# Performance work log

Hardware: AMD Instinct MI355X
Metric: run time of the kernel (lower is better)

## Reference

```python
import jax, jax.numpy as jnp
import numpy as np

N, E, G = 32768, 262144, 512
IN_DIM, HID, HEADS = 300, 128, 4
D_FUSED = HID * HEADS  # 512
L = 3


def setup_inputs() -> dict:
    key = jax.random.key(0)
    ks = jax.random.split(key, 24)
    s = 0.02
    inp = {
        "x": jax.random.normal(ks[0], (N, IN_DIM), jnp.float32),
        "edge_index": jax.random.randint(ks[1], (2, E), 0, N, jnp.int32),
        "batch": jnp.sort(jax.random.randint(ks[2], (N,), 0, G, jnp.int32)),
        "syn_w": jax.random.normal(ks[3], (IN_DIM, HID)) * s,
        "syn_b": jnp.zeros((HID,), jnp.float32),
        "ant_w": jax.random.normal(ks[4], (IN_DIM, HID)) * s,
        "ant_b": jnp.zeros((HID,), jnp.float32),
        "fusion_w": jax.random.normal(ks[5], (2 * HID, D_FUSED)) * s,
        "fusion_b": jnp.zeros((D_FUSED,), jnp.float32),
        "Wq": jax.random.normal(ks[6], (L, D_FUSED, D_FUSED)) * s,
        "bq": jnp.zeros((L, D_FUSED), jnp.float32),
        "Wk": jax.random.normal(ks[7], (L, D_FUSED, D_FUSED)) * s,
        "bk": jnp.zeros((L, D_FUSED), jnp.float32),
        "Wv": jax.random.normal(ks[8], (L, D_FUSED, D_FUSED)) * s,
        "bv": jnp.zeros((L, D_FUSED), jnp.float32),
        "Wskip": jax.random.normal(ks[9], (L, D_FUSED, D_FUSED)) * s,
        "bskip": jnp.zeros((L, D_FUSED), jnp.float32),
        "cls_w1": jax.random.normal(ks[10], (D_FUSED, HID)) * s,
        "cls_b1": jnp.zeros((HID,), jnp.float32),
        "cls_w2": jax.random.normal(ks[11], (HID, 1)) * s,
        "cls_b2": jnp.zeros((1,), jnp.float32),
    }
    return inp


def _transformer_conv(h, src, dst, Wq, bq, Wk, bk, Wv, bv, Wskip, bskip):
    # PyG TransformerConv: per-edge dot-product attention, softmax over in-neighbors of dst,
    # concat heads, plus root/skip linear (root_weight=True, concat=True, no edge_attr).
    n = h.shape[0]
    q = (h @ Wq + bq).reshape(n, HEADS, HID)
    k = (h @ Wk + bk).reshape(n, HEADS, HID)
    v = (h @ Wv + bv).reshape(n, HEADS, HID)
    scale = 1.0 / np.sqrt(HID)
    logits = jnp.einsum("ehd,ehd->eh", q[dst], k[src]) * scale  # [E, H]
    m = jax.ops.segment_max(logits, dst, num_segments=n)        # [N, H]
    e = jnp.exp(logits - m[dst])
    z = jax.ops.segment_sum(e, dst, num_segments=n)
    alpha = e / (z[dst] + 1e-16)                                # [E, H]
    msg = alpha[:, :, None] * v[src]                            # [E, H, D]
    out = jax.ops.segment_sum(msg, dst, num_segments=n).reshape(n, D_FUSED)
    return out + h @ Wskip + bskip


def reference(x, edge_index, batch, syn_w, syn_b, ant_w, ant_b, fusion_w, fusion_b,
              Wq, bq, Wk, bk, Wv, bv, Wskip, bskip, cls_w1, cls_b1, cls_w2, cls_b2):
    x_syn = jax.nn.relu(x @ syn_w + syn_b)
    x_ant = jax.nn.relu(x @ ant_w + ant_b)
    h = jnp.concatenate([x_syn, x_ant], axis=1) @ fusion_w + fusion_b  # [N, 512]
    src, dst = edge_index[0], edge_index[1]
    for l in range(L):
        h = jax.nn.relu(_transformer_conv(h, src, dst, Wq[l], bq[l], Wk[l], bk[l],
                                          Wv[l], bv[l], Wskip[l], bskip[l]))
    cnt = jax.ops.segment_sum(jnp.ones((h.shape[0],), h.dtype), batch, num_segments=G)
    pooled = jax.ops.segment_sum(h, batch, num_segments=G) / jnp.maximum(cnt, 1.0)[:, None]
    hid = jax.nn.relu(pooled @ cls_w1 + cls_b1)
    out = jax.nn.sigmoid(hid @ cls_w2 + cls_b2)
    return out.squeeze()
```

## Files before the change

kernel.cpp:

```cpp
#include <hip/hip_runtime.h>
#include <hip/hip_bf16.h>
#include <hip/hip_fp8.h>
#include <math.h>

#define N_NODES 32768
#define N_EDGES 262144
#define N_GRAPHS 512
#define IN_DIM 300
#define KPAD 320
#define HID 128
#define HEADS 4
#define D_FUSED 512
#define N_LAYERS 3

typedef __hip_bfloat16 bf16;
typedef short bf16x8 __attribute__((ext_vector_type(8)));
typedef short bf16x4 __attribute__((ext_vector_type(4)));
typedef float f32x4 __attribute__((ext_vector_type(4)));
typedef float f32x2 __attribute__((ext_vector_type(2)));

__device__ __forceinline__ float bfs_to_f(short s)
{
    unsigned u = ((unsigned)(unsigned short)s) << 16;
    return __builtin_bit_cast(float, u);
}

__device__ __forceinline__ short f_to_bfs(float v)
{
    return (short)__builtin_bit_cast(unsigned short, __float2bfloat16(v));
}

__device__ __forceinline__ void bf8_to_f32(bf16x8 v, float* f)
{
#pragma unroll
    for (int j = 0; j < 8; ++j) f[j] = bfs_to_f(v[j]);
}

__device__ __forceinline__ unsigned char f32_to_fp8(float v)
{
#if __has_builtin(__builtin_amdgcn_cvt_pk_fp8_f32)
    int p = __builtin_amdgcn_cvt_pk_fp8_f32(v, v, 0, false);
    return (unsigned char)(p & 0xff);
#else
    __hip_fp8_e4m3 t(v);
    return (unsigned char)t.__x;
#endif
}

__device__ __forceinline__ void fp8x8_to_f32(uint2 w, float* f)
{
#if __has_builtin(__builtin_amdgcn_cvt_pk_f32_fp8)
    f32x2 a = __builtin_amdgcn_cvt_pk_f32_fp8((int)w.x, false);
    f32x2 b = __builtin_amdgcn_cvt_pk_f32_fp8((int)w.x, true);
    f32x2 c = __builtin_amdgcn_cvt_pk_f32_fp8((int)w.y, false);
    f32x2 d = __builtin_amdgcn_cvt_pk_f32_fp8((int)w.y, true);
    f[0] = a.x; f[1] = a.y; f[2] = b.x; f[3] = b.y;
    f[4] = c.x; f[5] = c.y; f[6] = d.x; f[7] = d.y;
#else
    const unsigned char* p = (const unsigned char*)&w;
#pragma unroll
    for (int j = 0; j < 8; ++j) {
        __hip_fp8_e4m3 t;
        t.__x = (__hip_fp8_storage_t)p[j];
        f[j] = (float)t;
    }
#endif
}

__device__ __forceinline__ void gload_lds16(const void* g, void* l)
{
    __builtin_amdgcn_global_load_lds(
        (const __attribute__((address_space(1))) void*)g,
        (__attribute__((address_space(3))) void*)l, 16, 0, 0);
}

template <int K, int ACT, int EPI>
__global__ __launch_bounds__(512, 4) void mfma_gemm128(
    const bf16* __restrict__ A, int lda,
    const bf16* __restrict__ Bt,
    const float* __restrict__ bias,
    bf16* __restrict__ C0, int ldc0,
    bf16* __restrict__ C1, int ldc1, int csplit,
    unsigned char* __restrict__ C2,
    int nbx)
{
    __shared__ __align__(16) char lds[49152];

    const int t = threadIdx.x;
    const int wid = t >> 6, lane = t & 63;
    const int hi = lane >> 4, li = lane & 15;
    const int wr = wid >> 2, wc = wid & 3;

    int wg = blockIdx.x;
    if ((gridDim.x & 7) == 0) {
        const int cpx = gridDim.x >> 3;
        wg = (wg & 7) * cpx + (wg >> 3);
    }
    const int mb = wg / nbx, nb = wg % nbx;
    const int brow = mb * 128, bcol = nb * 256;
    constexpr int NT = K >> 5;

    const int rowA = t >> 2;
    const int slA = (((t & 3) ^ ((rowA >> 1) & 3)) * 8);
    const int cB1 = t + 512;
    const int rowB1 = cB1 >> 2;
    const int slB1 = (((cB1 & 3) ^ ((rowB1 >> 1) & 3)) * 8);

    const bf16* gA  = A  + (size_t)(brow + rowA)  * lda + slA;
    const bf16* gB0 = Bt + (size_t)(bcol + rowA)  * K   + slA;
    const bf16* gB1 = Bt + (size_t)(bcol + rowB1) * K   + slB1;

    auto stage = [&](int buf, int kt1) {
        const int ko = kt1 * 32;
        const int base = buf * 24576;
        gload_lds16(gA  + ko, lds + base + wid * 1024);
        gload_lds16(gB0 + ko, lds + base + 8192 + wid * 1024);
        gload_lds16(gB1 + ko, lds + base + 16384 + wid * 1024);
    };

    f32x4 acc[4][4] = {};

    stage(0, 0);

#pragma unroll
    for (int kt = 0; kt < NT; ++kt) {
        const int b = kt & 1;
        const char* Aslab = lds + b * 24576;
        const char* Bslab = Aslab + 8192;

        if (kt < NT - 1) {
            stage(b ^ 1, kt + 1);
            asm volatile("s_waitcnt vmcnt(3)" ::: "memory");
        } else {
            asm volatile("s_waitcnt vmcnt(0)" ::: "memory");
        }
        __builtin_amdgcn_s_barrier();
        __builtin_amdgcn_sched_barrier(0);

        bf16x8 bfrag[4];
#pragma unroll
        for (int n = 0; n < 4; ++n) {
            const int row = wc * 64 + n * 16 + li;
            bfrag[n] = *(const bf16x8*)(
                Bslab + row * 64 + ((hi ^ ((row >> 1) & 3)) << 4));
        }
        bf16x8 af[4];
#pragma unroll
        for (int m = 0; m < 4; ++m) {
            const int row = wr * 64 + m * 16 + li;
            af[m] = *(const bf16x8*)(
                Aslab + row * 64 + ((hi ^ ((row >> 1) & 3)) << 4));
        }
        __builtin_amdgcn_s_setprio(1);
#pragma unroll
        for (int m = 0; m < 4; ++m)
#pragma unroll
            for (int n = 0; n < 4; ++n)
                acc[m][n] = __builtin_amdgcn_mfma_f32_16x16x32_bf16(
                    af[m], bfrag[n], acc[m][n], 0, 0, 0);
        __builtin_amdgcn_s_setprio(0);

        __builtin_amdgcn_s_barrier();
        __builtin_amdgcn_sched_barrier(0);
    }

    if (EPI == 0) {
        const bool lo = (bcol < csplit);
        bf16* Cd = lo ? C0 : C1;
        const int ldc = lo ? ldc0 : ldc1;
        const int csub = lo ? 0 : csplit;
#pragma unroll
        for (int m = 0; m < 4; ++m)
#pragma unroll
            for (int n = 0; n < 4; ++n) {
                const int col = bcol + wc * 64 + n * 16 + li;
                const float bv = bias[col];
#pragma unroll
                for (int r = 0; r < 4; ++r) {
                    const int row = brow + wr * 64 + m * 16 + hi * 4 + r;
                    float v = acc[m][n][r] + bv;
                    if (ACT == 1) v = fmaxf(v, 0.f);
                    Cd[(size_t)row * ldc + (col - csub)] = __float2bfloat16(v);
                }
            }
    } else if (bcol < 512) {
#pragma unroll
        for (int m = 0; m < 4; ++m)
#pragma unroll
            for (int n = 0; n < 4; ++n) {
                const int col = bcol + wc * 64 + n * 16 + li;
                const float bv = bias[col];
#pragma unroll
                for (int r = 0; r < 4; ++r) {
                    const int row = brow + wr * 64 + m * 16 + hi * 4 + r;
                    C0[(size_t)row * ldc0 + col] = __float2bfloat16(acc[m][n][r] + bv);
                }
            }
    } else {
#pragma unroll
        for (int m = 0; m < 4; ++m)
#pragma unroll
            for (int n = 0; n < 4; ++n) {
                const int col = bcol + wc * 64 + n * 16 + li;
                const float bv = bias[col];
#pragma unroll
                for (int r = 0; r < 4; ++r) {
                    const int row = brow + wr * 64 + m * 16 + hi * 4 + r;
                    C2[(size_t)row * 1536 + (col - 512)] = f32_to_fp8(acc[m][n][r] + bv);
                }
            }
    }
}

template <int ACT>
__global__ __launch_bounds__(256) void mfma_gemm(
    const bf16* __restrict__ A, int lda,
    const bf16* __restrict__ Bt,
    const float* __restrict__ bias,
    bf16* __restrict__ C, int ldc, int K)
{
    __shared__ __align__(16) char lds[16384];
    char* As = lds;
    char* Bs = lds + 8192;

    const int t = threadIdx.x;
    const int wid = t >> 6, lane = t & 63;
    const int brow = blockIdx.x * 128;
    const int bcol = blockIdx.y * 128;
    const int wr = wid >> 1, wc = wid & 1;

    f32x4 acc[4][4] = {};

    for (int k0 = 0; k0 < K; k0 += 32) {
#pragma unroll
        for (int j = 0; j < 2; ++j) {
            const int seg = wid * 2 + j;
            const int row = seg * 16 + (lane >> 2);
            const int clin = lane & 3;
            const int clog = clin ^ ((row >> 1) & 3);
            gload_lds16(A + (size_t)(brow + row) * lda + k0 + clog * 8,
                        As + seg * 1024);
            gload_lds16(Bt + (size_t)(bcol + row) * K + k0 + clog * 8,
                        Bs + seg * 1024);
        }
        __syncthreads();

        bf16x8 af[4], bfr[4];
#pragma unroll
        for (int m = 0; m < 4; ++m) {
            const int row = wr * 64 + m * 16 + (lane & 15);
            const int cl = (lane >> 4) ^ ((row >> 1) & 3);
            af[m] = *(const bf16x8*)(As + row * 64 + cl * 16);
        }
#pragma unroll
        for (int n = 0; n < 4; ++n) {
            const int row = wc * 64 + n * 16 + (lane & 15);
            const int cl = (lane >> 4) ^ ((row >> 1) & 3);
            bfr[n] = *(const bf16x8*)(Bs + row * 64 + cl * 16);
        }
#pragma unroll
        for (int m = 0; m < 4; ++m)
#pragma unroll
            for (int n = 0; n < 4; ++n)
                acc[m][n] = __builtin_amdgcn_mfma_f32_16x16x32_bf16(
                    af[m], bfr[n], acc[m][n], 0, 0, 0);
        __syncthreads();
    }

#pragma unroll
    for (int m = 0; m < 4; ++m) {
#pragma unroll
        for (int n = 0; n < 4; ++n) {
            const int col = bcol + wc * 64 + n * 16 + (lane & 15);
            const float bv = bias[col];
#pragma unroll
            for (int r = 0; r < 4; ++r) {
                const int row = brow + wr * 64 + m * 16 + (lane >> 4) * 4 + r;
                float v = acc[m][n][r] + bv;
                if (ACT == 1) v = fmaxf(v, 0.f);
                C[(size_t)row * ldc + col] = __float2bfloat16(v);
            }
        }
    }
}

__global__ void prep_xpad_kernel(const float* __restrict__ x, bf16* __restrict__ xb)
{
    const int idx = blockIdx.x * 256 + threadIdx.x;
    const int n = idx / 80, q = idx % 80;
    bf16x4 o;
    if (q < 75) {
        const float4 v = *(const float4*)(x + (size_t)n * IN_DIM + q * 4);
        o[0] = f_to_bfs(v.x); o[1] = f_to_bfs(v.y);
        o[2] = f_to_bfs(v.z); o[3] = f_to_bfs(v.w);
    } else {
        o[0] = 0; o[1] = 0; o[2] = 0; o[3] = 0;
    }
    *(bf16x4*)(xb + (size_t)n * KPAD + q * 4) = o;
}

__global__ void prep_encw_kernel(const float* __restrict__ syn_w,
                                 const float* __restrict__ ant_w,
                                 bf16* __restrict__ wt)
{
    const int c = blockIdx.x, k = threadIdx.x;
    float v = 0.f;
    if (k < IN_DIM) v = (c < HID) ? syn_w[k * HID + c] : ant_w[k * HID + (c - HID)];
    wt[c * KPAD + k] = __float2bfloat16(v);
}

__global__ void prep_fusw_kernel(const float* __restrict__ fw, bf16* __restrict__ wt)
{
    const int c = blockIdx.x, k = threadIdx.x;
    wt[c * 256 + k] = __float2bfloat16(fw[k * D_FUSED + c]);
}

__global__ __launch_bounds__(256) void prep_combw_kernel(
    const float* __restrict__ Wskip,
    const float* __restrict__ Wq,
    const float* __restrict__ Wk,
    const float* __restrict__ Wv,
    bf16* __restrict__ wt)
{
    __shared__ float tile[32][33];
    const int blk = blockIdx.x;
    const int l = blk >> 10, rem = blk & 1023;
    const int cb = rem >> 4, kb = rem & 15;
    const int c0 = cb * 32;

    const int sel = c0 >> 9;
    const float* mat = (sel == 0) ? Wskip : (sel == 1) ? Wq : (sel == 2) ? Wk : Wv;
    const int cp0 = c0 & 511;

    const int j = threadIdx.x & 31;
    const int i0 = threadIdx.x >> 5;
#pragma unroll
    for (int s = 0; s < 4; ++s) {
        const int i = i0 + 8 * s;
        tile[i][j] = mat[((size_t)l * 512 + kb * 32 + i) * 512 + cp0 + j];
    }
    __syncthreads();
#pragma unroll
    for (int s = 0; s < 4; ++s) {
        const int jj = i0 + 8 * s;
        wt[((size_t)l * 2048 + c0 + jj) * 512 + kb * 32 + j] =
            __float2bfloat16(tile[j][jj]);
    }
}

__global__ void prep_bias_kernel(const float* __restrict__ syn_b,
                                 const float* __restrict__ ant_b,
                                 const float* __restrict__ bskip,
                                 const float* __restrict__ bq,
                                 const float* __restrict__ bk,
                                 const float* __restrict__ bv,
                                 float* __restrict__ benc,
                                 float* __restrict__ bcomb)
{
    const int i = blockIdx.x * 256 + threadIdx.x;
    if (i < 256) benc[i] = (i < HID) ? syn_b[i] : ant_b[i - HID];
    const int j = i - 256;
    if (j >= 0 && j < 6144) {
        const int l = j >> 11, c = j & 2047;
        const int sel = c >> 9, col = c & 511;
        const float* s = (sel == 0) ? bskip : (sel == 1) ? bq : (sel == 2) ? bk : bv;
        bcomb[j] = s[l * D_FUSED + col];
    }
}

__global__ void zero_int_kernel(int* __restrict__ p, int n)
{
    int i = blockIdx.x * 256 + threadIdx.x;
    if (i < n) p[i] = 0;
}

__global__ void hist_kernel(const int* __restrict__ dst, int* __restrict__ deg, int E)
{
    int e = blockIdx.x * 256 + threadIdx.x;
    if (e < E) atomicAdd(&deg[dst[e]], 1);
}

__global__ __launch_bounds__(256) void partial_sum_kernel(const int* __restrict__ deg,
                                                          int* __restrict__ part)
{
    int v = deg[blockIdx.x * 256 + threadIdx.x];
#pragma unroll
    for (int o = 32; o; o >>= 1) v += __shfl_xor(v, o);
    __shared__ int w4[4];
    if ((threadIdx.x & 63) == 0) w4[threadIdx.x >> 6] = v;
    __syncthreads();
    if (threadIdx.x == 0) part[blockIdx.x] = w4[0] + w4[1] + w4[2] + w4[3];
}

__global__ __launch_bounds__(128) void scan_part_kernel(int* __restrict__ part)
{
    __shared__ int s[128];
    const int t = threadIdx.x;
    s[t] = part[t];
    __syncthreads();
    for (int o = 1; o < 128; o <<= 1) {
        int v = (t >= o) ? s[t - o] : 0;
        __syncthreads();
        s[t] += v;
        __syncthreads();
    }
    part[t] = (t == 0) ? 0 : s[t - 1];
}

__global__ __launch_bounds__(256) void off_kernel(const int* __restrict__ deg,
                                                  const int* __restrict__ part,
                                                  int* __restrict__ off)
{
    __shared__ int s[256];
    const int b = blockIdx.x, t = threadIdx.x;
    s[t] = deg[b * 256 + t];
    __syncthreads();
    for (int o = 1; o < 256; o <<= 1) {
        int v = (t >= o) ? s[t - o] : 0;
        __syncthreads();
        s[t] += v;
        __syncthreads();
    }
    const int excl = (t == 0) ? 0 : s[t - 1];
    off[b * 256 + t] = part[b] + excl;
    if (b == 127 && t == 255) off[N_NODES] = part[127] + s[255];
}

__global__ void scatter_kernel(const int* __restrict__ src, const int* __restrict__ dst,
                               const int* __restrict__ off, int* __restrict__ cursor,
                               int* __restrict__ csr_src, int E)
{
    int e = blockIdx.x * 256 + threadIdx.x;
    if (e < E) {
        int d = dst[e];
        int pos = atomicAdd(&cursor[d], 1);
        csr_src[off[d] + pos] = src[e];
    }
}

__global__ __launch_bounds__(256) void attn_kernel(
    const unsigned char* __restrict__ qkvb, bf16* __restrict__ hout,
    const int* __restrict__ off, const int* __restrict__ csr)
{
    const int n = blockIdx.x;
    const int hd = threadIdx.x >> 6;
    const int lane = threadIdx.x & 63;
    const int g = lane >> 4, sub = lane & 15;
    const float scale = 0.08838834764831845f;

    float qf[8];
    fp8x8_to_f32(*(const uint2*)(qkvb + (size_t)n * 1536 + hd * 128 + sub * 8), qf);

    float zA = 0.f, zB = 0.f;
    float accA[8] = {}, accB[8] = {};

    const int s0 = off[n], s1 = off[n + 1];
    for (int e0 = s0; e0 < s1; e0 += 8) {
        const int ea = e0 + g;
        const int eb = e0 + 4 + g;
        const bool va = (ea < s1);
        const bool vb = (eb < s1);
        const int sa = va ? csr[ea] : 0;
        const int sb = vb ? csr[eb] : 0;
        const unsigned char* pa = qkvb + (size_t)sa * 1536 + hd * 128 + sub * 8;
        const unsigned char* pb = qkvb + (size_t)sb * 1536 + hd * 128 + sub * 8;

        const uint2 kwa = *(const uint2*)(pa + 512);
        const uint2 kwb = *(const uint2*)(pb + 512);
        const uint2 vwa = *(const uint2*)(pa + 1024);
        const uint2 vwb = *(const uint2*)(pb + 1024);

        float kfa[8], kfb[8];
        fp8x8_to_f32(kwa, kfa);
        fp8x8_to_f32(kwb, kfb);
        float da = 0.f, db = 0.f;
#pragma unroll
        for (int j = 0; j < 8; ++j) {
            da = fmaf(qf[j], kfa[j], da);
            db = fmaf(qf[j], kfb[j], db);
        }
        da += __shfl_xor(da, 1);  db += __shfl_xor(db, 1);
        da += __shfl_xor(da, 2);  db += __shfl_xor(db, 2);
        da += __shfl_xor(da, 4);  db += __shfl_xor(db, 4);
        da += __shfl_xor(da, 8);  db += __shfl_xor(db, 8);

        const float wa = va ? __expf(da * scale) : 0.f;
        const float wb = vb ? __expf(db * scale) : 0.f;
        zA += wa;
        zB += wb;

        float vfa[8], vfb[8];
        fp8x8_to_f32(vwa, vfa);
        fp8x8_to_f32(vwb, vfb);
#pragma unroll
        for (int j = 0; j < 8; ++j) {
            accA[j] = fmaf(wa, vfa[j], accA[j]);
            accB[j] = fmaf(wb, vfb[j], accB[j]);
        }
    }

    float zz = zA + zB;
    zz += __shfl_xor(zz, 16);
    zz += __shfl_xor(zz, 32);
    const float inv = 1.f / (zz + 1e-16f);

    float o[8];
#pragma unroll
    for (int j = 0; j < 8; ++j) {
        float a = accA[j] + accB[j];
        a += __shfl_xor(a, 16);
        a += __shfl_xor(a, 32);
        o[j] = a * inv;
    }

    if (g == 0) {
        const size_t ob = (size_t)n * D_FUSED + hd * HID + sub * 8;
        const bf16x8 sk = *(const bf16x8*)(hout + ob);
        bf16x8 res;
#pragma unroll
        for (int j = 0; j < 8; ++j)
            res[j] = f_to_bfs(fmaxf(o[j] + bfs_to_f(sk[j]), 0.f));
        *(bf16x8*)(hout + ob) = res;
    }
}

__global__ __launch_bounds__(256) void pool_kernel(const bf16* __restrict__ h,
                                                   const int* __restrict__ batch,
                                                   float* __restrict__ pooled)
{
    const int g = blockIdx.x;
    int a = 0, b = N_NODES;
    while (a < b) { int mid = (a + b) >> 1; if (batch[mid] < g) a = mid + 1; else b = mid; }
    const int start = a;
    b = N_NODES;
    while (a < b) { int mid = (a + b) >> 1; if (batch[mid] < g + 1) a = mid + 1; else b = mid; }
    const int end = a;
    const float invc = 1.f / fmaxf((float)(end - start), 1.f);

    const int nl = threadIdx.x >> 6;
    const int dl = threadIdx.x & 63;

    float s[8] = {};
    for (int nidx = start + nl; nidx < end; nidx += 4) {
        const bf16x8 v = *(const bf16x8*)(h + (size_t)nidx * D_FUSED + dl * 8);
#pragma unroll
        for (int j = 0; j < 8; ++j) s[j] += bfs_to_f(v[j]);
    }

    __shared__ float red[4][512];
#pragma unroll
    for (int j = 0; j < 8; ++j) red[nl][dl * 8 + j] = s[j];
    __syncthreads();
    if (nl == 0) {
#pragma unroll
        for (int j = 0; j < 8; ++j) {
            const int d = dl * 8 + j;
            pooled[(size_t)g * D_FUSED + d] =
                (red[0][d] + red[1][d] + red[2][d] + red[3][d]) * invc;
        }
    }
}

__global__ __launch_bounds__(128) void cls_kernel(const float* __restrict__ pooled,
                                                  const float* __restrict__ w1,
                                                  const float* __restrict__ b1,
                                                  const float* __restrict__ w2,
                                                  const float* __restrict__ b2,
                                                  float* __restrict__ out)
{
    const int g = blockIdx.x;
    const int j = threadIdx.x;
    const float* p = pooled + (size_t)g * D_FUSED;
    float acc = 0.f;
    for (int i = 0; i < D_FUSED; ++i) acc += p[i] * w1[i * HID + j];
    const float hid = fmaxf(acc + b1[j], 0.f);
    float val = hid * w2[j];
#pragma unroll
    for (int o = 32; o; o >>= 1) val += __shfl_xor(val, o);
    __shared__ float ws2[2];
    if ((threadIdx.x & 63) == 0) ws2[threadIdx.x >> 6] = val;
    __syncthreads();
    if (threadIdx.x == 0) {
        const float sum = ws2[0] + ws2[1] + b2[0];
        out[g] = 1.f / (1.f + __expf(-sum));
    }
}

extern "C" void kernel_launch(void* const* d_in, const int* in_sizes, int n_in,
                              void* d_out, int out_size, void* d_ws, size_t ws_size,
                              hipStream_t stream)
{
    const float* x        = (const float*)d_in[0];
    const int*   ei       = (const int*)d_in[1];
    const int*   batch    = (const int*)d_in[2];
    const float* syn_w    = (const float*)d_in[3];
    const float* syn_b    = (const float*)d_in[4];
    const float* ant_w    = (const float*)d_in[5];
    const float* ant_b    = (const float*)d_in[6];
    const float* fusion_w = (const float*)d_in[7];
    const float* fusion_b = (const float*)d_in[8];
    const float* Wq       = (const float*)d_in[9];
    const float* bq       = (const float*)d_in[10];
    const float* Wk       = (const float*)d_in[11];
    const float* bk       = (const float*)d_in[12];
    const float* Wv       = (const float*)d_in[13];
    const float* bv       = (const float*)d_in[14];
    const float* Wskip    = (const float*)d_in[15];
    const float* bskip    = (const float*)d_in[16];
    const float* cls_w1   = (const float*)d_in[17];
    const float* cls_b1   = (const float*)d_in[18];
    const float* cls_w2   = (const float*)d_in[19];
    const float* cls_b2   = (const float*)d_in[20];

    const int* src = ei;
    const int* dst = ei + N_EDGES;

    const size_t NV = (size_t)N_NODES * D_FUSED;
    bf16* hA    = (bf16*)d_ws;
    bf16* hB    = hA + NV;
    unsigned char* qkv = (unsigned char*)(hB + NV);
    bf16* wenc  = (bf16*)(qkv + (size_t)N_NODES * 1536);
    bf16* wfus  = wenc + 256 * KPAD;
    bf16* wcomb = wfus + 512 * 256;
    float* benc = (float*)(wcomb + (size_t)3 * 2048 * 512);
    float* bcomb = benc + 256;
    float* pooled = bcomb + 6144;
    int* deg    = (int*)(pooled + (size_t)N_GRAPHS * D_FUSED);
    int* cursor = deg + N_NODES;
    int* part   = cursor + N_NODES;
    int* off    = part + 128;
    int* csr    = off + N_NODES + 1;

    bf16* xb   = (bf16*)qkv;
    bf16* tenc = hB;

    zero_int_kernel<<<(2 * N_NODES + 255) / 256, 256, 0, stream>>>(deg, 2 * N_NODES);
    hist_kernel<<<N_EDGES / 256, 256, 0, stream>>>(dst, deg, N_EDGES);
    partial_sum_kernel<<<128, 256, 0, stream>>>(deg, part);
    scan_part_kernel<<<1, 128, 0, stream>>>(part);
    off_kernel<<<128, 256, 0, stream>>>(deg, part, off);
    scatter_kernel<<<N_EDGES / 256, 256, 0, stream>>>(src, dst, off, cursor, csr, N_EDGES);

    prep_xpad_kernel<<<(N_NODES * 80) / 256, 256, 0, stream>>>(x, xb);
    prep_encw_kernel<<<256, KPAD, 0, stream>>>(syn_w, ant_w, wenc);
    prep_fusw_kernel<<<512, 256, 0, stream>>>(fusion_w, wfus);
    prep_combw_kernel<<<3072, 256, 0, stream>>>(Wskip, Wq, Wk, Wv, wcomb);
    prep_bias_kernel<<<25, 256, 0, stream>>>(syn_b, ant_b, bskip, bq, bk, bv, benc, bcomb);

    mfma_gemm<1><<<dim3(N_NODES / 128, 2), 256, 0, stream>>>(
        xb, KPAD, wenc, benc, tenc, 256, KPAD);
    mfma_gemm128<256, 0, 0><<<512, 512, 0, stream>>>(
        tenc, 256, wfus, fusion_b, hA, D_FUSED, hA, D_FUSED, D_FUSED, nullptr, 2);

    bf16* hcur = hA;
    bf16* hnew = hB;
    for (int l = 0; l < N_LAYERS; ++l) {
        mfma_gemm128<512, 0, 1><<<2048, 512, 0, stream>>>(
            hcur, D_FUSED, wcomb + (size_t)l * 2048 * D_FUSED,
            bcomb + (size_t)l * 2048,
            hnew, D_FUSED, nullptr, 0, 512, qkv, 8);
        attn_kernel<<<N_NODES, 256, 0, stream>>>(qkv, hnew, off, csr);
        bf16* tmp = hcur; hcur = hnew; hnew = tmp;
    }

    pool_kernel<<<N_GRAPHS, 256, 0, stream>>>(hcur, batch, pooled);
    cls_kernel<<<N_GRAPHS, 128, 0, stream>>>(pooled, cls_w1, cls_b1, cls_w2, cls_b2,
                                             (float*)d_out);
}
```

Measured before the change: 579.7 us.

## Triple-buffer GEMM LDS pipeline, fuse pool with classifier, zero cursor in scan

The 128x256 MFMA GEMM moves from double to triple buffering in LDS (72KB), prefetching two k-tiles ahead with adjusted vmcnt waits to better hide global-to-LDS latency. The pooling and classifier kernels are merged into one kernel that keeps pooled features in shared memory, removing a launch and a global round trip. Cursor zeroing moves into the offset kernel, which halves the zero kernel. The larger LDS footprint may reduce occupancy of the GEMM at 512 threads per block.

```diff
diff --git a/kernel.cpp b/kernel.cpp
--- a/kernel.cpp
+++ b/kernel.cpp
@@ -84,7 +84,7 @@
     unsigned char* __restrict__ C2,
     int nbx)
 {
-    __shared__ __align__(16) char lds[49152];
+    __shared__ __align__(16) char lds[73728];
 
     const int t = threadIdx.x;
     const int wid = t >> 6, lane = t & 63;
@@ -121,15 +121,18 @@
     f32x4 acc[4][4] = {};
 
     stage(0, 0);
+    if (NT > 1) stage(1, 1);
 
 #pragma unroll
     for (int kt = 0; kt < NT; ++kt) {
-        const int b = kt & 1;
+        const int b = kt % 3;
         const char* Aslab = lds + b * 24576;
         const char* Bslab = Aslab + 8192;
 
-        if (kt < NT - 1) {
-            stage(b ^ 1, kt + 1);
+        if (kt < NT - 2) {
+            stage((kt + 2) % 3, kt + 2);
+            asm volatile("s_waitcnt vmcnt(6)" ::: "memory");
+        } else if (kt == NT - 2) {
             asm volatile("s_waitcnt vmcnt(3)" ::: "memory");
         } else {
             asm volatile("s_waitcnt vmcnt(0)" ::: "memory");
@@ -409,11 +412,13 @@
 
 __global__ __launch_bounds__(256) void off_kernel(const int* __restrict__ deg,
                                                   const int* __restrict__ part,
-                                                  int* __restrict__ off)
+                                                  int* __restrict__ off,
+                                                  int* __restrict__ cursor)
 {
     __shared__ int s[256];
     const int b = blockIdx.x, t = threadIdx.x;
     s[t] = deg[b * 256 + t];
+    cursor[b * 256 + t] = 0;
     __syncthreads();
     for (int o = 1; o < 256; o <<= 1) {
         int v = (t >= o) ? s[t - o] : 0;
@@ -524,9 +529,11 @@
     }
 }
 
-__global__ __launch_bounds__(256) void pool_kernel(const bf16* __restrict__ h,
-                                                   const int* __restrict__ batch,
-                                                   float* __restrict__ pooled)
+__global__ __launch_bounds__(256) void pool_cls_kernel(
+    const bf16* __restrict__ h, const int* __restrict__ batch,
+    const float* __restrict__ w1, const float* __restrict__ b1,
+    const float* __restrict__ w2, const float* __restrict__ b2,
+    float* __restrict__ out)
 {
     const int g = blockIdx.x;
     int a = 0, b = N_NODES;
@@ -548,6 +555,7 @@
     }
 
     __shared__ float red[4][512];
+    __shared__ float pooled[512];
 #pragma unroll
     for (int j = 0; j < 8; ++j) red[nl][dl * 8 + j] = s[j];
     __syncthreads();
@@ -555,30 +563,23 @@
 #pragma unroll
         for (int j = 0; j < 8; ++j) {
             const int d = dl * 8 + j;
-            pooled[(size_t)g * D_FUSED + d] =
-                (red[0][d] + red[1][d] + red[2][d] + red[3][d]) * invc;
-        }
-    }
-}
-
-__global__ __launch_bounds__(128) void cls_kernel(const float* __restrict__ pooled,
-                                                  const float* __restrict__ w1,
-                                                  const float* __restrict__ b1,
-                                                  const float* __restrict__ w2,
-                                                  const float* __restrict__ b2,
-                                                  float* __restrict__ out)
-{
-    const int g = blockIdx.x;
-    const int j = threadIdx.x;
-    const float* p = pooled + (size_t)g * D_FUSED;
-    float acc = 0.f;
-    for (int i = 0; i < D_FUSED; ++i) acc += p[i] * w1[i * HID + j];
-    const float hid = fmaxf(acc + b1[j], 0.f);
-    float val = hid * w2[j];
+            pooled[d] = (red[0][d] + red[1][d] + red[2][d] + red[3][d]) * invc;
+        }
+    }
+    __syncthreads();
+
+    float val = 0.f;
+    if (threadIdx.x < 128) {
+        const int j = threadIdx.x;
+        float acc = 0.f;
+        for (int i = 0; i < D_FUSED; ++i) acc = fmaf(pooled[i], w1[i * HID + j], acc);
+        const float hid = fmaxf(acc + b1[j], 0.f);
+        val = hid * w2[j];
+    }
 #pragma unroll
     for (int o = 32; o; o >>= 1) val += __shfl_xor(val, o);
     __shared__ float ws2[2];
-    if ((threadIdx.x & 63) == 0) ws2[threadIdx.x >> 6] = val;
+    if ((threadIdx.x & 63) == 0 && threadIdx.x < 128) ws2[threadIdx.x >> 6] = val;
     __syncthreads();
     if (threadIdx.x == 0) {
         const float sum = ws2[0] + ws2[1] + b2[0];
@@ -624,8 +625,7 @@
     bf16* wcomb = wfus + 512 * 256;
     float* benc = (float*)(wcomb + (size_t)3 * 2048 * 512);
     float* bcomb = benc + 256;
-    float* pooled = bcomb + 6144;
-    int* deg    = (int*)(pooled + (size_t)N_GRAPHS * D_FUSED);
+    int* deg    = (int*)(bcomb + 6144);
     int* cursor = deg + N_NODES;
     int* part   = cursor + N_NODES;
     int* off    = part + 128;
@@ -634,11 +634,11 @@
     bf16* xb   = (bf16*)qkv;
     bf16* tenc = hB;
 
-    zero_int_kernel<<<(2 * N_NODES + 255) / 256, 256, 0, stream>>>(deg, 2 * N_NODES);
+    zero_int_kernel<<<(N_NODES + 255) / 256, 256, 0, stream>>>(deg, N_NODES);
     hist_kernel<<<N_EDGES / 256, 256, 0, stream>>>(dst, deg, N_EDGES);
     partial_sum_kernel<<<128, 256, 0, stream>>>(deg, part);
     scan_part_kernel<<<1, 128, 0, stream>>>(part);
-    off_kernel<<<128, 256, 0, stream>>>(deg, part, off);
+    off_kernel<<<128, 256, 0, stream>>>(deg, part, off, cursor);
     scatter_kernel<<<N_EDGES / 256, 256, 0, stream>>>(src, dst, off, cursor, csr, N_EDGES);
 
     prep_xpad_kernel<<<(N_NODES * 80) / 256, 256, 0, stream>>>(x, xb);
@@ -663,7 +663,6 @@
         bf16* tmp = hcur; hcur = hnew; hnew = tmp;
     }
 
-    pool_kernel<<<N_GRAPHS, 256, 0, stream>>>(hcur, batch, pooled);
-    cls_kernel<<<N_GRAPHS, 128, 0, stream>>>(pooled, cls_w1, cls_b1, cls_w2, cls_b2,
-                                             (float*)d_out);
-}
+    pool_cls_kernel<<<N_GRAPHS, 256, 0, stream>>>(hcur, batch, cls_w1, cls_b1,
+                                                  cls_w2, cls_b2, (float*)d_out);
+}
```

Result: faster. 554.4 us (-4.4%).
